# Optimization experiments

Measured on AMD Instinct MI355X. Metric: run time of the kernel, lower is better.

The kernel has to match this reference:

```python
import jax, jax.numpy as jnp
import numpy as np

EPS = 1e-5
NUM_HEADS = 8


def _ln(x, w, b):
    m = x.mean(-1, keepdims=True)
    v = jnp.mean(jnp.square(x - m), -1, keepdims=True)
    return (x - m) * jax.lax.rsqrt(v + EPS) * w + b


def _bn(x, w, b, mean, var):  # x: [N, C, T], eval-mode BatchNorm1d
    return (x - mean[None, :, None]) * jax.lax.rsqrt(var[None, :, None] + EPS) * w[None, :, None] + b[None, :, None]


def setup_inputs() -> dict:
    key = jax.random.key(0)
    ks = jax.random.split(key, 32)
    B, T, E, C = 8, 64, 128, 256
    H = 2 * C       # temporal conv hidden
    M = 4 * C       # mlp hidden
    s = 0.02
    f32 = jnp.float32
    inp = {
        'x': jax.random.normal(ks[0], (B, T, E, C), f32),
        'adj_mask': jax.random.randint(ks[1], (E, E), 0, 2, jnp.int32),
        'n1_w': 1.0 + s * jax.random.normal(ks[2], (C,), f32),
        'n1_b': s * jax.random.normal(ks[3], (C,), f32),
        'q_w': s * jax.random.normal(ks[4], (C, C), f32),
        'k_w': s * jax.random.normal(ks[5], (C, C), f32),
        'v_w': s * jax.random.normal(ks[6], (C, C), f32),
        'proj_w': s * jax.random.normal(ks[7], (C, C), f32),
        'proj_b': s * jax.random.normal(ks[8], (C,), f32),
        'on_w': 1.0 + s * jax.random.normal(ks[9], (C,), f32),
        'on_b': s * jax.random.normal(ks[10], (C,), f32),
        'gamma_s': jnp.asarray([0.5], f32),
        'conv1_w': s * jax.random.normal(ks[11], (H, C, 3), f32),
        'bn1_w': 1.0 + s * jax.random.normal(ks[12], (H,), f32),
        'bn1_b': s * jax.random.normal(ks[13], (H,), f32),
        'bn1_m': s * jax.random.normal(ks[14], (H,), f32),
        'bn1_v': jax.random.uniform(ks[15], (H,), f32, 0.5, 1.5),
        'conv2_w': s * jax.random.normal(ks[16], (C, H, 1), f32),
        'bn2_w': 1.0 + s * jax.random.normal(ks[17], (C,), f32),
        'bn2_b': s * jax.random.normal(ks[18], (C,), f32),
        'bn2_m': s * jax.random.normal(ks[19], (C,), f32),
        'bn2_v': jax.random.uniform(ks[20], (C,), f32, 0.5, 1.5),
        'tn_w': 1.0 + s * jax.random.normal(ks[21], (C,), f32),
        'tn_b': s * jax.random.normal(ks[22], (C,), f32),
        'gamma_t': jnp.asarray([0.5], f32),
        'n3_w': 1.0 + s * jax.random.normal(ks[23], (C,), f32),
        'n3_b': s * jax.random.normal(ks[24], (C,), f32),
        'fc1_w': s * jax.random.normal(ks[25], (C, M), f32),
        'fc1_b': s * jax.random.normal(ks[26], (M,), f32),
        'fc2_w': s * jax.random.normal(ks[27], (M, C), f32),
        'fc2_b': s * jax.random.normal(ks[28], (C,), f32),
    }
    return inp


def reference(x, adj_mask, n1_w, n1_b, q_w, k_w, v_w, proj_w, proj_b, on_w, on_b,
              gamma_s, conv1_w, bn1_w, bn1_b, bn1_m, bn1_v, conv2_w, bn2_w, bn2_b,
              bn2_m, bn2_v, tn_w, tn_b, gamma_t, n3_w, n3_b, fc1_w, fc1_b, fc2_w, fc2_b):
    B, T, E, C = x.shape
    Hh = NUM_HEADS
    D = C // Hh
    mask = adj_mask.astype(x.dtype)

    # ---- spatial geometric-cosine attention (per frame) ----
    xs = _ln(x, n1_w, n1_b)                                   # norm1
    q = (xs @ q_w).reshape(B, T, E, Hh, D)
    k = (xs @ k_w).reshape(B, T, E, Hh, D)
    v = (xs @ v_w).reshape(B, T, E, Hh, D)
    attn = jnp.einsum('btehd,btfhd->bthef', q, k)             # [B,T,H,E,E]
    attn = (attn * mask[None, None, None] + 1.0) * 0.5        # affine mask, no softmax
    o = jnp.einsum('bthef,btfhd->btehd', attn, v).reshape(B, T, E, C)
    o = _ln(o @ proj_w + proj_b, on_w, on_b)                  # proj + output_norm
    x = x + (xs + gamma_s * o)                                # inner + outer residual

    # ---- temporal convolution (norm2 is Identity) ----
    xt = _ln(x, tn_w, tn_b)
    xc = xt.transpose(0, 2, 3, 1).reshape(B * E, C, T)        # 'b t e c -> (b e) c t'
    dn = ('NCH', 'OIH', 'NCH')
    y = jax.lax.conv_general_dilated(xc, conv1_w, (1,), [(1, 1)], dimension_numbers=dn)
    y = jax.nn.gelu(_bn(y, bn1_w, bn1_b, bn1_m, bn1_v), approximate=False)
    y = jax.lax.conv_general_dilated(y, conv2_w, (1,), [(0, 0)], dimension_numbers=dn)
    y = _bn(y, bn2_w, bn2_b, bn2_m, bn2_v)
    y = y.reshape(B, E, C, T).transpose(0, 3, 1, 2)           # '(b e) c t -> b t e c'
    x = x + (x + gamma_t * y)                                 # temporal inner + outer residual

    # ---- MLP ----
    xm = _ln(x, n3_w, n3_b)
    h = jax.nn.gelu(xm @ fc1_w + fc1_b, approximate=False)
    x = x + (h @ fc2_w + fc2_b)
    return x
```

## Files before the change

kernel.cpp:

```cpp
#include <hip/hip_runtime.h>
#include <cstdint>

constexpr int Bn = 8, Tn = 64, En = 128, Cn = 256;
constexpr int Hn = 512, Mn = 1024, NHd = 8, Dn = 32;
constexpr int NTOK = Bn * Tn * En;
constexpr size_t SZ = (size_t)NTOK * Cn;
#define EPSF 1e-5f

typedef __attribute__((ext_vector_type(8))) short short8;
typedef __attribute__((ext_vector_type(4))) float f32x4;

__device__ __forceinline__ float bf2f(unsigned short u) {
  union { unsigned int i; float f; } c; c.i = ((unsigned int)u) << 16; return c.f;
}
__device__ __forceinline__ unsigned short f2bf(float f) {
  union { float f; unsigned int i; } c; c.f = f;
  unsigned int u = c.i;
  return (unsigned short)((u + 0x7fffu + ((u >> 16) & 1u)) >> 16);
}
__device__ __forceinline__ float gelu_f(float v) {
  float x2 = v * v;
  float p = v * fmaf(x2, 0.10294532f, 2.30221000f);
  float d = 1.0f + __builtin_amdgcn_exp2f(-p);
  return v * __builtin_amdgcn_rcpf(d);
}

__device__ __forceinline__ void gload16(const unsigned short* g, unsigned short* l) {
  __builtin_amdgcn_global_load_lds(
      (const __attribute__((address_space(1))) unsigned int*)g,
      (__attribute__((address_space(3))) unsigned int*)l, 16, 0, 0);
}

#define MEMFENCE() asm volatile("" ::: "memory")

template <int EPI, bool C1A>
__global__ __launch_bounds__(512) void mfma_gemm(
    const unsigned short* __restrict__ A,
    const unsigned short* __restrict__ Bt,
    const float* __restrict__ scale,
    const float* __restrict__ bias,
    const float* __restrict__ resf,
    const float* __restrict__ gscal,
    void* __restrict__ outv,
    int K, int N) {
  __shared__ unsigned short lds[4][2][8192];
  int tid = threadIdx.x;
  int lane = tid & 63, wave = tid >> 6;
  int wr = wave >> 2, wc = wave & 3;

  int nwg = gridDim.x * gridDim.y;
  int flat = blockIdx.y * gridDim.x + blockIdx.x;
  int cpx = nwg >> 3;
  int swz = (flat & 7) * cpx + (flat >> 3);
  int ntile = swz % gridDim.x;
  int mtile = swz / gridDim.x;
  int rowBase = mtile * 256;
  int colBase = ntile * 256;
  int lda = C1A ? 256 : K;

  int arow = lane & 15, g8 = (lane >> 4) * 8;
  int aoff[8], boff[4];
#pragma unroll
  for (int m = 0; m < 8; ++m) aoff[m] = (wr * 128 + m * 16 + arow) * 32 + g8;
#pragma unroll
  for (int n = 0; n < 4; ++n) boff[n] = (wc * 64 + n * 16 + arow) * 32 + g8;

  f32x4 acc[8][4];
#pragma unroll
  for (int m = 0; m < 8; ++m)
#pragma unroll
    for (int n = 0; n < 4; ++n) acc[m][n] = (f32x4)(0.0f);

  int srow = lane >> 2;
  int scol = (lane & 3) * 8;

  auto stageA = [&](int T) {
    int k0 = T << 5, slot = T & 3;
#pragma unroll
    for (int r = 0; r < 2; ++r) {
      int row = r * 128 + wave * 16 + srow;
      const unsigned short* src;
      if (C1A) {
        int idx = rowBase + row;
        int bb = idx >> 13, tt = (idx >> 7) & 63, e = idx & 127;
        src = A + ((size_t)((bb * 66 + tt + (k0 >> 8)) * 128 + e)) * 256 +
              (k0 & 255) + scol;
      } else {
        src = A + (size_t)(rowBase + row) * lda + k0 + scol;
      }
      gload16(src, &lds[slot][0][r * 4096 + wave * 512]);
    }
  };
  auto stageB = [&](int T) {
    int k0 = T << 5, slot = T & 3;
#pragma unroll
    for (int r = 0; r < 2; ++r) {
      int row = r * 128 + wave * 16 + srow;
      const unsigned short* src = Bt + (size_t)(colBase + row) * K + k0 + scol;
      gload16(src, &lds[slot][1][r * 4096 + wave * 512]);
    }
  };

  auto tile = [&](int T, int vm, bool st) {
    if (vm == 8)      asm volatile("s_waitcnt vmcnt(8)" ::: "memory");
    else if (vm == 4) asm volatile("s_waitcnt vmcnt(4)" ::: "memory");
    else              asm volatile("s_waitcnt vmcnt(0)" ::: "memory");
    __builtin_amdgcn_sched_barrier(0);
    __builtin_amdgcn_s_barrier();
    MEMFENCE();
    if (st) stageA(T + 3);
    const unsigned short* as = &lds[T & 3][0][0];
    const unsigned short* bs = &lds[T & 3][1][0];
    short8 bfr[4], af[4];
#pragma unroll
    for (int n = 0; n < 4; ++n) bfr[n] = *(const short8*)(bs + boff[n]);
#pragma unroll
    for (int m = 0; m < 4; ++m) af[m] = *(const short8*)(as + aoff[m]);
    __builtin_amdgcn_s_setprio(1);
#pragma unroll
    for (int m = 0; m < 4; ++m)
#pragma unroll
      for (int n = 0; n < 4; ++n)
        acc[m][n] = __builtin_amdgcn_mfma_f32_16x16x32_bf16(af[m], bfr[n], acc[m][n], 0, 0, 0);
    __builtin_amdgcn_s_setprio(0);
    if (st) stageB(T + 3);
#pragma unroll
    for (int m = 0; m < 4; ++m) af[m] = *(const short8*)(as + aoff[4 + m]);
    __builtin_amdgcn_s_setprio(1);
#pragma unroll
    for (int m = 0; m < 4; ++m)
#pragma unroll
      for (int n = 0; n < 4; ++n)
        acc[4 + m][n] = __builtin_amdgcn_mfma_f32_16x16x32_bf16(af[m], bfr[n], acc[4 + m][n], 0, 0, 0);
    __builtin_amdgcn_s_setprio(0);
  };

  stageA(0); stageB(0); stageA(1); stageB(1); stageA(2); stageB(2);
  int nkt = K >> 5;
  for (int T = 0; T < nkt - 3; ++T) tile(T, 8, true);
  tile(nkt - 3, 8, false);
  tile(nkt - 2, 4, false);
  tile(nkt - 1, 0, false);
  MEMFENCE();

  int crow0 = (lane >> 4) * 4, ccol = lane & 15;
  size_t rb = (size_t)rowBase + wr * 128;
  int cb = colBase + wc * 64;
  float gt = (EPI == 3) ? gscal[0] : 0.f;
  float bi[4], sc[4];
#pragma unroll
  for (int n = 0; n < 4; ++n) {
    int col = cb + n * 16 + ccol;
    bi[n] = (EPI >= 1 && bias) ? bias[col] : 0.f;
    sc[n] = ((EPI == 2 || EPI == 3) && scale) ? scale[col] : 1.f;
  }
#pragma unroll
  for (int m = 0; m < 8; ++m) {
#pragma unroll
    for (int n = 0; n < 4; ++n) {
      int col = cb + n * 16 + ccol;
#pragma unroll
      for (int r = 0; r < 4; ++r) {
        size_t row = rb + m * 16 + crow0 + r;
        size_t idx = row * (size_t)N + col;
        float v = acc[m][n][r];
        if (EPI == 0)      ((unsigned short*)outv)[idx] = f2bf(v);
        else if (EPI == 1) ((unsigned short*)outv)[idx] = f2bf(v + bi[n]);
        else if (EPI == 2) ((unsigned short*)outv)[idx] = f2bf(gelu_f(v * sc[n] + bi[n]));
        else if (EPI == 3) ((float*)outv)[idx] = 2.0f * resf[idx] + gt * (v * sc[n] + bi[n]);
        else if (EPI == 4) ((float*)outv)[idx] = resf[idx] + v + bi[n];
        else if (EPI == 5) ((float*)outv)[idx] = v + bi[n];
      }
    }
  }
}

template <bool PAD>
__global__ __launch_bounds__(256) void ln256_bf(const float* __restrict__ src,
                                                const float* __restrict__ w,
                                                const float* __restrict__ b,
                                                unsigned short* __restrict__ dst) {
  int lane = threadIdx.x & 63;
  int tok = blockIdx.x * 4 + (threadIdx.x >> 6);
  const float4* row = (const float4*)(src + (size_t)tok * Cn);
  float4 v = row[lane];
  float s  = v.x + v.y + v.z + v.w;
  float s2 = v.x*v.x + v.y*v.y + v.z*v.z + v.w*v.w;
#pragma unroll
  for (int off = 32; off >= 1; off >>= 1) {
    s  += __shfl_xor(s, off, 64);
    s2 += __shfl_xor(s2, off, 64);
  }
  float mean = s * (1.0f / Cn);
  float var = fmaxf(s2 * (1.0f / Cn) - mean * mean, 0.0f);
  float r = rsqrtf(var + EPSF);
  float4 wv = ((const float4*)w)[lane];
  float4 bv = ((const float4*)b)[lane];
  size_t dtok = tok;
  if (PAD) {
    int bb = tok >> 13, tt = (tok >> 7) & 63, e = tok & 127;
    dtok = ((size_t)(bb * 66 + tt + 1)) * 128 + e;
  }
  ushort4 o;
  o.x = f2bf((v.x - mean) * r * wv.x + bv.x);
  o.y = f2bf((v.y - mean) * r * wv.y + bv.y);
  o.z = f2bf((v.z - mean) * r * wv.z + bv.z);
  o.w = f2bf((v.w - mean) * r * wv.w + bv.w);
  *(ushort4*)(dst + dtok * Cn + lane * 4) = o;
}

__global__ __launch_bounds__(256) void attn_mfma(const unsigned short* __restrict__ qkv,
                                                 const float* __restrict__ maskh,
                                                 unsigned short* __restrict__ o) {
  __shared__ unsigned short Qs[128 * 32];
  __shared__ unsigned short Ks[128 * 32];
  __shared__ unsigned short Vt[32 * 136];
  __shared__ unsigned short Ps[128 * 136];
  int tid = threadIdx.x, lane = tid & 63, wave = tid >> 6;
  int h = blockIdx.x & 7, bt = blockIdx.x >> 3;
  size_t gbase = (size_t)bt * 128 * 768 + h * 32;
#pragma unroll
  for (int i = 0; i < 2; ++i) {
    int q = wave * 2 + i;
    int row = q * 16 + (lane >> 2);
    int seg = (lane & 3) * 8;
    gload16(qkv + gbase + (size_t)row * 768 + seg, &Qs[q * 512]);
    gload16(qkv + gbase + 256 + (size_t)row * 768 + seg, &Ks[q * 512]);
  }
  {
    int e = tid >> 1, dh = (tid & 1) * 16;
    const unsigned short* gv = qkv + gbase + 512 + (size_t)e * 768 + dh;
    short8 v0 = *(const short8*)gv;
    short8 v1 = *(const short8*)(gv + 8);
#pragma unroll
    for (int j = 0; j < 8; ++j) {
      Vt[(dh + j) * 136 + e]     = (unsigned short)v0[j];
      Vt[(dh + 8 + j) * 136 + e] = (unsigned short)v1[j];
    }
  }
  __syncthreads();
  int arow = lane & 15, akk = (lane >> 4) * 8;
  int crow0 = (lane >> 4) * 4, ccol = lane & 15;
  short8 af0 = *(const short8*)&Qs[(wave * 32 + arow) * 32 + akk];
  short8 af1 = *(const short8*)&Qs[(wave * 32 + 16 + arow) * 32 + akk];
#pragma unroll
  for (int j = 0; j < 8; ++j) {
    short8 bfr = *(const short8*)&Ks[(j * 16 + arow) * 32 + akk];
    f32x4 s0 = __builtin_amdgcn_mfma_f32_16x16x32_bf16(af0, bfr, (f32x4)(0.0f), 0, 0, 0);
    f32x4 s1 = __builtin_amdgcn_mfma_f32_16x16x32_bf16(af1, bfr, (f32x4)(0.0f), 0, 0, 0);
    int f = j * 16 + ccol;
#pragma unroll
    for (int r = 0; r < 4; ++r) {
      int e0 = wave * 32 + crow0 + r;
      int e1 = e0 + 16;
      Ps[e0 * 136 + f] = f2bf(maskh[e0 * 128 + f] * s0[r] + 0.5f);
      Ps[e1 * 136 + f] = f2bf(maskh[e1 * 128 + f] * s1[r] + 0.5f);
    }
  }
  f32x4 acc[2][2];
#pragma unroll
  for (int i = 0; i < 2; ++i)
#pragma unroll
    for (int j = 0; j < 2; ++j) acc[i][j] = (f32x4)(0.0f);
#pragma unroll
  for (int k0 = 0; k0 < 128; k0 += 32) {
    short8 a0 = *(const short8*)&Ps[(wave * 32 + arow) * 136 + k0 + akk];
    short8 a1 = *(const short8*)&Ps[(wave * 32 + 16 + arow) * 136 + k0 + akk];
    short8 b0 = *(const short8*)&Vt[arow * 136 + k0 + akk];
    short8 b1 = *(const short8*)&Vt[(16 + arow) * 136 + k0 + akk];
    acc[0][0] = __builtin_amdgcn_mfma_f32_16x16x32_bf16(a0, b0, acc[0][0], 0, 0, 0);
    acc[0][1] = __builtin_amdgcn_mfma_f32_16x16x32_bf16(a0, b1, acc[0][1], 0, 0, 0);
    acc[1][0] = __builtin_amdgcn_mfma_f32_16x16x32_bf16(a1, b0, acc[1][0], 0, 0, 0);
    acc[1][1] = __builtin_amdgcn_mfma_f32_16x16x32_bf16(a1, b1, acc[1][1], 0, 0, 0);
  }
  unsigned short* ob = o + (size_t)bt * 128 * 256 + h * 32;
#pragma unroll
  for (int i = 0; i < 2; ++i)
#pragma unroll
    for (int j = 0; j < 2; ++j)
#pragma unroll
      for (int r = 0; r < 4; ++r) {
        int e = wave * 32 + i * 16 + crow0 + r;
        ob[(size_t)e * 256 + j * 16 + ccol] = f2bf(acc[i][j][r]);
      }
}

__global__ __launch_bounds__(256) void resid1_kernel(const float* __restrict__ x,
                                                     const unsigned short* __restrict__ xs,
                                                     const unsigned short* __restrict__ p2,
                                                     const float* __restrict__ gs,
                                                     float* __restrict__ x1) {
  size_t i = ((size_t)blockIdx.x * 256 + threadIdx.x) * 4;
  float g = gs[0];
  float4 xv = *(const float4*)(x + i);
  ushort4 s4 = *(const ushort4*)(xs + i);
  ushort4 p4 = *(const ushort4*)(p2 + i);
  float4 r;
  r.x = xv.x + bf2f(s4.x) + g * bf2f(p4.x);
  r.y = xv.y + bf2f(s4.y) + g * bf2f(p4.y);
  r.z = xv.z + bf2f(s4.z) + g * bf2f(p4.z);
  r.w = xv.w + bf2f(s4.w) + g * bf2f(p4.w);
  *(float4*)(x1 + i) = r;
}

__global__ __launch_bounds__(256) void transcast(const float* __restrict__ src,
                                                 unsigned short* __restrict__ dst,
                                                 int N, int K) {
  int idx = blockIdx.x * 256 + threadIdx.x;
  int n = idx / K, k = idx - n * K;
  dst[idx] = f2bf(src[(size_t)k * N + n]);
}
__global__ __launch_bounds__(256) void castbf(const float* __restrict__ s,
                                              unsigned short* __restrict__ d) {
  int i = blockIdx.x * 256 + threadIdx.x;
  d[i] = f2bf(s[i]);
}
__global__ __launch_bounds__(256) void pack_conv1(const float* __restrict__ w1,
                                                  unsigned short* __restrict__ dst) {
  int idx = blockIdx.x * 256 + threadIdx.x;
  int hh = idx / 768, kk = idx - hh * 768;
  int slab = kk >> 8, c = kk & 255;
  dst[idx] = f2bf(w1[(size_t)hh * 768 + c * 3 + slab]);
}
__global__ __launch_bounds__(256) void bnfold(const float* __restrict__ w,
                                              const float* __restrict__ bvec,
                                              const float* __restrict__ m,
                                              const float* __restrict__ v,
                                              float* __restrict__ s,
                                              float* __restrict__ o, int n) {
  int i = blockIdx.x * 256 + threadIdx.x;
  if (i < n) {
    float sc = w[i] * rsqrtf(v[i] + EPSF);
    s[i] = sc;
    o[i] = bvec[i] - m[i] * sc;
  }
}
__global__ __launch_bounds__(256) void mask_prep(const int* __restrict__ adj,
                                                 float* __restrict__ maskh) {
  int i = blockIdx.x * 256 + threadIdx.x;
  maskh[i] = 0.5f * (float)adj[i];
}
__global__ __launch_bounds__(256) void zero_pad(unsigned short* __restrict__ xt) {
  int idx = blockIdx.x * 256 + threadIdx.x;
  int bb = idx >> 16;
  int rem = idx & 65535;
  int which = rem >> 15;
  int off = rem & 32767;
  size_t base = ((size_t)(bb * 66 + which * 65)) * 128 * 256;
  xt[base + off] = 0;
}

extern "C" void kernel_launch(void* const* d_in, const int* in_sizes, int n_in,
                              void* d_out, int out_size, void* d_ws, size_t ws_size,
                              hipStream_t stream) {
  (void)in_sizes; (void)n_in; (void)out_size; (void)ws_size;
  const float* x       = (const float*)d_in[0];
  const int*   adj     = (const int*)  d_in[1];
  const float* n1_w    = (const float*)d_in[2];
  const float* n1_b    = (const float*)d_in[3];
  const float* q_w     = (const float*)d_in[4];
  const float* k_w     = (const float*)d_in[5];
  const float* v_w     = (const float*)d_in[6];
  const float* proj_w  = (const float*)d_in[7];
  const float* proj_b  = (const float*)d_in[8];
  const float* on_w    = (const float*)d_in[9];
  const float* on_b    = (const float*)d_in[10];
  const float* gamma_s = (const float*)d_in[11];
  const float* conv1_w = (const float*)d_in[12];
  const float* bn1_w   = (const float*)d_in[13];
  const float* bn1_b   = (const float*)d_in[14];
  const float* bn1_m   = (const float*)d_in[15];
  const float* bn1_v   = (const float*)d_in[16];
  const float* conv2_w = (const float*)d_in[17];
  const float* bn2_w   = (const float*)d_in[18];
  const float* bn2_b   = (const float*)d_in[19];
  const float* bn2_m   = (const float*)d_in[20];
  const float* bn2_v   = (const float*)d_in[21];
  const float* tn_w    = (const float*)d_in[22];
  const float* tn_b    = (const float*)d_in[23];
  const float* gamma_t = (const float*)d_in[24];
  const float* n3_w    = (const float*)d_in[25];
  const float* n3_b    = (const float*)d_in[26];
  const float* fc1_w   = (const float*)d_in[27];
  const float* fc1_b   = (const float*)d_in[28];
  const float* fc2_w   = (const float*)d_in[29];
  const float* fc2_b   = (const float*)d_in[30];
  float* O = (float*)d_out;

  const size_t MB = 1024 * 1024;
  char* wsb = (char*)d_ws;
  unsigned short* qkvb = (unsigned short*)(wsb + 0);
  float*          pjo  = (float*)(wsb + 0);
  float*          x1b  = (float*)(wsb + 0);
  unsigned short* xmb  = (unsigned short*)(wsb + 0);
  unsigned short* hb   = (unsigned short*)(wsb + 32 * MB);
  unsigned short* xtp  = (unsigned short*)(wsb + 64 * MB);
  unsigned short* xsb  = (unsigned short*)(wsb + 96 * MB);
  unsigned short* oat  = (unsigned short*)(wsb + 128 * MB);
  unsigned short* p2b  = (unsigned short*)(wsb + 128 * MB);
  unsigned short* y1b  = (unsigned short*)(wsb + 100 * MB);
  char* wp = wsb + 164 * MB;
  unsigned short* Wqkv = (unsigned short*)wp;  wp += 768 * 256 * 2;
  unsigned short* PjT  = (unsigned short*)wp;  wp += 256 * 256 * 2;
  unsigned short* W1t  = (unsigned short*)wp;  wp += 512 * 768 * 2;
  unsigned short* W2t  = (unsigned short*)wp;  wp += 256 * 512 * 2;
  unsigned short* F1t  = (unsigned short*)wp;  wp += 1024 * 256 * 2;
  unsigned short* F2t  = (unsigned short*)wp;  wp += 256 * 1024 * 2;
  float* s1 = (float*)wp; wp += 512 * 4;
  float* o1 = (float*)wp; wp += 512 * 4;
  float* s2 = (float*)wp; wp += 256 * 4;
  float* o2 = (float*)wp; wp += 256 * 4;
  float* maskh = (float*)wp; wp += 16384 * 4;

  transcast<<<768 * 256 / 256, 256, 0, stream>>>(q_w, Wqkv, 256, 256);
  transcast<<<768 * 256 / 256, 256, 0, stream>>>(k_w, Wqkv + 256 * 256, 256, 256);
  transcast<<<768 * 256 / 256, 256, 0, stream>>>(v_w, Wqkv + 512 * 256, 256, 256);
  transcast<<<256 * 256 / 256, 256, 0, stream>>>(proj_w, PjT, 256, 256);
  pack_conv1<<<512 * 768 / 256, 256, 0, stream>>>(conv1_w, W1t);
  castbf<<<256 * 512 / 256, 256, 0, stream>>>(conv2_w, W2t);
  transcast<<<1024 * 256 / 256, 256, 0, stream>>>(fc1_w, F1t, 1024, 256);
  transcast<<<256 * 1024 / 256, 256, 0, stream>>>(fc2_w, F2t, 256, 1024);
  bnfold<<<2, 256, 0, stream>>>(bn1_w, bn1_b, bn1_m, bn1_v, s1, o1, 512);
  bnfold<<<1, 256, 0, stream>>>(bn2_w, bn2_b, bn2_m, bn2_v, s2, o2, 256);
  mask_prep<<<64, 256, 0, stream>>>(adj, maskh);
  zero_pad<<<524288 / 256, 256, 0, stream>>>(xtp);

  ln256_bf<false><<<NTOK / 4, 256, 0, stream>>>(x, n1_w, n1_b, xsb);
  mfma_gemm<0, false><<<dim3(3, 256), 512, 0, stream>>>(xsb, Wqkv, nullptr, nullptr, nullptr, nullptr, qkvb, 256, 768);
  attn_mfma<<<Bn * Tn * NHd, 256, 0, stream>>>(qkvb, maskh, oat);
  mfma_gemm<5, false><<<dim3(1, 256), 512, 0, stream>>>(oat, PjT, nullptr, proj_b, nullptr, nullptr, pjo, 256, 256);
  ln256_bf<false><<<NTOK / 4, 256, 0, stream>>>(pjo, on_w, on_b, p2b);
  resid1_kernel<<<(int)(SZ / (4 * 256)), 256, 0, stream>>>(x, xsb, p2b, gamma_s, x1b);

  ln256_bf<true><<<NTOK / 4, 256, 0, stream>>>(x1b, tn_w, tn_b, xtp);
  mfma_gemm<2, true><<<dim3(2, 256), 512, 0, stream>>>(xtp, W1t, s1, o1, nullptr, nullptr, y1b, 768, 512);
  mfma_gemm<3, false><<<dim3(1, 256), 512, 0, stream>>>(y1b, W2t, s2, o2, x1b, gamma_t, O, 512, 256);

  ln256_bf<false><<<NTOK / 4, 256, 0, stream>>>(O, n3_w, n3_b, xmb);
  mfma_gemm<2, false><<<dim3(4, 256), 512, 0, stream>>>(xmb, F1t, nullptr, fc1_b, nullptr, nullptr, hb, 256, 1024);
  mfma_gemm<4, false><<<dim3(1, 256), 512, 0, stream>>>(hb, F2t, nullptr, fc2_b, O, nullptr, O, 1024, 256);
}
```

Before: 607.5 us.

## Transpose MFMA operands for vectorized epilogue stores and fuse output LN with residual

```diff
diff --git a/kernel.cpp b/kernel.cpp
--- a/kernel.cpp
+++ b/kernel.cpp
@@ -33,7 +33,7 @@
 
 #define MEMFENCE() asm volatile("" ::: "memory")
 
-template <int EPI, bool C1A>
+template <int EPI, bool C1A, int KT, int NT>
 __global__ __launch_bounds__(512) void mfma_gemm(
     const unsigned short* __restrict__ A,
     const unsigned short* __restrict__ Bt,
@@ -41,8 +41,7 @@
     const float* __restrict__ bias,
     const float* __restrict__ resf,
     const float* __restrict__ gscal,
-    void* __restrict__ outv,
-    int K, int N) {
+    void* __restrict__ outv) {
   __shared__ unsigned short lds[4][2][8192];
   int tid = threadIdx.x;
   int lane = tid & 63, wave = tid >> 6;
@@ -56,7 +55,7 @@
   int mtile = swz / gridDim.x;
   int rowBase = mtile * 256;
   int colBase = ntile * 256;
-  int lda = C1A ? 256 : K;
+  constexpr int lda = C1A ? 256 : KT;
 
   int arow = lane & 15, g8 = (lane >> 4) * 8;
   int aoff[8], boff[4];
@@ -96,7 +95,7 @@
 #pragma unroll
     for (int r = 0; r < 2; ++r) {
       int row = r * 128 + wave * 16 + srow;
-      const unsigned short* src = Bt + (size_t)(colBase + row) * K + k0 + scol;
+      const unsigned short* src = Bt + (size_t)(colBase + row) * KT + k0 + scol;
       gload16(src, &lds[slot][1][r * 4096 + wave * 512]);
     }
   };
@@ -121,7 +120,7 @@
     for (int m = 0; m < 4; ++m)
 #pragma unroll
       for (int n = 0; n < 4; ++n)
-        acc[m][n] = __builtin_amdgcn_mfma_f32_16x16x32_bf16(af[m], bfr[n], acc[m][n], 0, 0, 0);
+        acc[m][n] = __builtin_amdgcn_mfma_f32_16x16x32_bf16(bfr[n], af[m], acc[m][n], 0, 0, 0);
     __builtin_amdgcn_s_setprio(0);
     if (st) stageB(T + 3);
 #pragma unroll
@@ -131,45 +130,77 @@
     for (int m = 0; m < 4; ++m)
 #pragma unroll
       for (int n = 0; n < 4; ++n)
-        acc[4 + m][n] = __builtin_amdgcn_mfma_f32_16x16x32_bf16(af[m], bfr[n], acc[4 + m][n], 0, 0, 0);
+        acc[4 + m][n] = __builtin_amdgcn_mfma_f32_16x16x32_bf16(bfr[n], af[m], acc[4 + m][n], 0, 0, 0);
     __builtin_amdgcn_s_setprio(0);
   };
 
   stageA(0); stageB(0); stageA(1); stageB(1); stageA(2); stageB(2);
-  int nkt = K >> 5;
+  constexpr int nkt = KT >> 5;
+#pragma clang loop unroll(disable)
   for (int T = 0; T < nkt - 3; ++T) tile(T, 8, true);
   tile(nkt - 3, 8, false);
   tile(nkt - 2, 4, false);
   tile(nkt - 1, 0, false);
   MEMFENCE();
 
-  int crow0 = (lane >> 4) * 4, ccol = lane & 15;
+  int cm = lane & 15;
+  int cn0 = (lane >> 4) * 4;
   size_t rb = (size_t)rowBase + wr * 128;
   int cb = colBase + wc * 64;
   float gt = (EPI == 3) ? gscal[0] : 0.f;
-  float bi[4], sc[4];
+  float4 bi4[4], sc4[4];
 #pragma unroll
   for (int n = 0; n < 4; ++n) {
-    int col = cb + n * 16 + ccol;
-    bi[n] = (EPI >= 1 && bias) ? bias[col] : 0.f;
-    sc[n] = ((EPI == 2 || EPI == 3) && scale) ? scale[col] : 1.f;
+    int col = cb + n * 16 + cn0;
+    if (EPI != 0) bi4[n] = *(const float4*)(bias + col);
+    if (EPI == 2 || EPI == 3) {
+      if (scale) sc4[n] = *(const float4*)(scale + col);
+      else { sc4[n].x = 1.f; sc4[n].y = 1.f; sc4[n].z = 1.f; sc4[n].w = 1.f; }
+    }
   }
 #pragma unroll
   for (int m = 0; m < 8; ++m) {
+    size_t rowoff = (rb + m * 16 + cm) * (size_t)NT;
 #pragma unroll
     for (int n = 0; n < 4; ++n) {
-      int col = cb + n * 16 + ccol;
-#pragma unroll
-      for (int r = 0; r < 4; ++r) {
-        size_t row = rb + m * 16 + crow0 + r;
-        size_t idx = row * (size_t)N + col;
-        float v = acc[m][n][r];
-        if (EPI == 0)      ((unsigned short*)outv)[idx] = f2bf(v);
-        else if (EPI == 1) ((unsigned short*)outv)[idx] = f2bf(v + bi[n]);
-        else if (EPI == 2) ((unsigned short*)outv)[idx] = f2bf(gelu_f(v * sc[n] + bi[n]));
-        else if (EPI == 3) ((float*)outv)[idx] = 2.0f * resf[idx] + gt * (v * sc[n] + bi[n]);
-        else if (EPI == 4) ((float*)outv)[idx] = resf[idx] + v + bi[n];
-        else if (EPI == 5) ((float*)outv)[idx] = v + bi[n];
+      int col = cb + n * 16 + cn0;
+      f32x4 v = acc[m][n];
+      if (EPI == 0) {
+        ushort4 o = { f2bf(v[0]), f2bf(v[1]), f2bf(v[2]), f2bf(v[3]) };
+        *(ushort4*)((unsigned short*)outv + rowoff + col) = o;
+      } else if (EPI == 1) {
+        ushort4 o = { f2bf(v[0] + bi4[n].x), f2bf(v[1] + bi4[n].y),
+                      f2bf(v[2] + bi4[n].z), f2bf(v[3] + bi4[n].w) };
+        *(ushort4*)((unsigned short*)outv + rowoff + col) = o;
+      } else if (EPI == 2) {
+        ushort4 o = { f2bf(gelu_f(v[0] * sc4[n].x + bi4[n].x)),
+                      f2bf(gelu_f(v[1] * sc4[n].y + bi4[n].y)),
+                      f2bf(gelu_f(v[2] * sc4[n].z + bi4[n].z)),
+                      f2bf(gelu_f(v[3] * sc4[n].w + bi4[n].w)) };
+        *(ushort4*)((unsigned short*)outv + rowoff + col) = o;
+      } else if (EPI == 3) {
+        float4 rf = *(const float4*)(resf + rowoff + col);
+        float4 o;
+        o.x = 2.0f * rf.x + gt * (v[0] * sc4[n].x + bi4[n].x);
+        o.y = 2.0f * rf.y + gt * (v[1] * sc4[n].y + bi4[n].y);
+        o.z = 2.0f * rf.z + gt * (v[2] * sc4[n].z + bi4[n].z);
+        o.w = 2.0f * rf.w + gt * (v[3] * sc4[n].w + bi4[n].w);
+        *(float4*)((float*)outv + rowoff + col) = o;
+      } else if (EPI == 4) {
+        float4 rf = *(const float4*)(resf + rowoff + col);
+        float4 o;
+        o.x = rf.x + v[0] + bi4[n].x;
+        o.y = rf.y + v[1] + bi4[n].y;
+        o.z = rf.z + v[2] + bi4[n].z;
+        o.w = rf.w + v[3] + bi4[n].w;
+        *(float4*)((float*)outv + rowoff + col) = o;
+      } else if (EPI == 5) {
+        float4 o;
+        o.x = v[0] + bi4[n].x;
+        o.y = v[1] + bi4[n].y;
+        o.z = v[2] + bi4[n].z;
+        o.w = v[3] + bi4[n].w;
+        *(float4*)((float*)outv + rowoff + col) = o;
       }
     }
   }
@@ -209,6 +240,40 @@
   *(ushort4*)(dst + dtok * Cn + lane * 4) = o;
 }
 
+__global__ __launch_bounds__(256) void ln_resid(const float* __restrict__ pjo,
+                                                const float* __restrict__ w,
+                                                const float* __restrict__ b,
+                                                const float* __restrict__ x,
+                                                const unsigned short* __restrict__ xs,
+                                                const float* __restrict__ gs,
+                                                float* __restrict__ x1) {
+  int lane = threadIdx.x & 63;
+  int tok = blockIdx.x * 4 + (threadIdx.x >> 6);
+  size_t base = (size_t)tok * Cn;
+  float4 v = ((const float4*)(pjo + base))[lane];
+  float s  = v.x + v.y + v.z + v.w;
+  float s2 = v.x*v.x + v.y*v.y + v.z*v.z + v.w*v.w;
+#pragma unroll
+  for (int off = 32; off >= 1; off >>= 1) {
+    s  += __shfl_xor(s, off, 64);
+    s2 += __shfl_xor(s2, off, 64);
+  }
+  float mean = s * (1.0f / Cn);
+  float var = fmaxf(s2 * (1.0f / Cn) - mean * mean, 0.0f);
+  float r = rsqrtf(var + EPSF);
+  float4 wv = ((const float4*)w)[lane];
+  float4 bv = ((const float4*)b)[lane];
+  float g = gs[0];
+  float4 xv = ((const float4*)(x + base))[lane];
+  ushort4 s4 = ((const ushort4*)(xs + base))[lane];
+  float4 o;
+  o.x = xv.x + bf2f(s4.x) + g * ((v.x - mean) * r * wv.x + bv.x);
+  o.y = xv.y + bf2f(s4.y) + g * ((v.y - mean) * r * wv.y + bv.y);
+  o.z = xv.z + bf2f(s4.z) + g * ((v.z - mean) * r * wv.z + bv.z);
+  o.w = xv.w + bf2f(s4.w) + g * ((v.w - mean) * r * wv.w + bv.w);
+  ((float4*)(x1 + base))[lane] = o;
+}
+
 __global__ __launch_bounds__(256) void attn_mfma(const unsigned short* __restrict__ qkv,
                                                  const float* __restrict__ maskh,
                                                  unsigned short* __restrict__ o) {
@@ -283,24 +348,6 @@
         int e = wave * 32 + i * 16 + crow0 + r;
         ob[(size_t)e * 256 + j * 16 + ccol] = f2bf(acc[i][j][r]);
       }
-}
-
-__global__ __launch_bounds__(256) void resid1_kernel(const float* __restrict__ x,
-                                                     const unsigned short* __restrict__ xs,
-                                                     const unsigned short* __restrict__ p2,
-                                                     const float* __restrict__ gs,
-                                                     float* __restrict__ x1) {
-  size_t i = ((size_t)blockIdx.x * 256 + threadIdx.x) * 4;
-  float g = gs[0];
-  float4 xv = *(const float4*)(x + i);
-  ushort4 s4 = *(const ushort4*)(xs + i);
-  ushort4 p4 = *(const ushort4*)(p2 + i);
-  float4 r;
-  r.x = xv.x + bf2f(s4.x) + g * bf2f(p4.x);
-  r.y = xv.y + bf2f(s4.y) + g * bf2f(p4.y);
-  r.z = xv.z + bf2f(s4.z) + g * bf2f(p4.z);
-  r.w = xv.w + bf2f(s4.w) + g * bf2f(p4.w);
-  *(float4*)(x1 + i) = r;
 }
 
 __global__ __launch_bounds__(256) void transcast(const float* __restrict__ src,
@@ -397,7 +444,6 @@
   unsigned short* xtp  = (unsigned short*)(wsb + 64 * MB);
   unsigned short* xsb  = (unsigned short*)(wsb + 96 * MB);
   unsigned short* oat  = (unsigned short*)(wsb + 128 * MB);
-  unsigned short* p2b  = (unsigned short*)(wsb + 128 * MB);
   unsigned short* y1b  = (unsigned short*)(wsb + 100 * MB);
   char* wp = wsb + 164 * MB;
   unsigned short* Wqkv = (unsigned short*)wp;  wp += 768 * 256 * 2;
@@ -426,17 +472,16 @@
   zero_pad<<<524288 / 256, 256, 0, stream>>>(xtp);
 
   ln256_bf<false><<<NTOK / 4, 256, 0, stream>>>(x, n1_w, n1_b, xsb);
-  mfma_gemm<0, false><<<dim3(3, 256), 512, 0, stream>>>(xsb, Wqkv, nullptr, nullptr, nullptr, nullptr, qkvb, 256, 768);
+  mfma_gemm<0, false, 256, 768><<<dim3(3, 256), 512, 0, stream>>>(xsb, Wqkv, nullptr, nullptr, nullptr, nullptr, qkvb);
   attn_mfma<<<Bn * Tn * NHd, 256, 0, stream>>>(qkvb, maskh, oat);
-  mfma_gemm<5, false><<<dim3(1, 256), 512, 0, stream>>>(oat, PjT, nullptr, proj_b, nullptr, nullptr, pjo, 256, 256);
-  ln256_bf<false><<<NTOK / 4, 256, 0, stream>>>(pjo, on_w, on_b, p2b);
-  resid1_kernel<<<(int)(SZ / (4 * 256)), 256, 0, stream>>>(x, xsb, p2b, gamma_s, x1b);
+  mfma_gemm<5, false, 256, 256><<<dim3(1, 256), 512, 0, stream>>>(oat, PjT, nullptr, proj_b, nullptr, nullptr, pjo);
+  ln_resid<<<NTOK / 4, 256, 0, stream>>>(pjo, on_w, on_b, x, xsb, gamma_s, x1b);
 
   ln256_bf<true><<<NTOK / 4, 256, 0, stream>>>(x1b, tn_w, tn_b, xtp);
-  mfma_gemm<2, true><<<dim3(2, 256), 512, 0, stream>>>(xtp, W1t, s1, o1, nullptr, nullptr, y1b, 768, 512);
-  mfma_gemm<3, false><<<dim3(1, 256), 512, 0, stream>>>(y1b, W2t, s2, o2, x1b, gamma_t, O, 512, 256);
+  mfma_gemm<2, true, 768, 512><<<dim3(2, 256), 512, 0, stream>>>(xtp, W1t, s1, o1, nullptr, nullptr, y1b);
+  mfma_gemm<3, false, 512, 256><<<dim3(1, 256), 512, 0, stream>>>(y1b, W2t, s2, o2, x1b, gamma_t, O);
 
   ln256_bf<false><<<NTOK / 4, 256, 0, stream>>>(O, n3_w, n3_b, xmb);
-  mfma_gemm<2, false><<<dim3(4, 256), 512, 0, stream>>>(xmb, F1t, nullptr, fc1_b, nullptr, nullptr, hb, 256, 1024);
-  mfma_gemm<4, false><<<dim3(1, 256), 512, 0, stream>>>(hb, F2t, nullptr, fc2_b, O, nullptr, O, 1024, 256);
-}
+  mfma_gemm<2, false, 256, 1024><<<dim3(4, 256), 512, 0, stream>>>(xmb, F1t, nullptr, fc1_b, nullptr, nullptr, hb);
+  mfma_gemm<4, false, 1024, 256><<<dim3(1, 256), 512, 0, stream>>>(hb, F2t, nullptr, fc2_b, O, nullptr, O);
+}
```

Result: no change. 615.1 us (+1.2%).
